# Kernel optimization log

Measured on AMD Instinct MI355X. Metric: run time of the kernel, lower is better.

The kernel has to match this reference:

```python
import jax, jax.numpy as jnp
import numpy as np

B, S, E, L = 4, 4096, 1024, 64
SCALE = float(np.sqrt(L))


def setup_inputs() -> dict:
    key = jax.random.key(0)
    ks = jax.random.split(key, 7)
    x = jax.random.normal(ks[0], (B, S, E), dtype=jnp.float32)
    # causal mask: positions with mask==0 are disallowed (masked_fill semantics)
    mask = jnp.tril(jnp.ones((S, S), dtype=jnp.int32))
    # Linear params (torch Linear: y = x @ W.T + b); store as [E, L] for x @ W
    sd = 1.0 / np.sqrt(E)
    Wq = jax.random.uniform(ks[1], (E, L), jnp.float32, -sd, sd)
    Wk = jax.random.uniform(ks[2], (E, L), jnp.float32, -sd, sd)
    Wv = jax.random.uniform(ks[3], (E, L), jnp.float32, -sd, sd)
    bq = jax.random.uniform(ks[4], (L,), jnp.float32, -sd, sd)
    bk = jax.random.uniform(ks[5], (L,), jnp.float32, -sd, sd)
    bv = jax.random.uniform(ks[6], (L,), jnp.float32, -sd, sd)
    return {"x": x, "Wq": Wq, "Wk": Wk, "Wv": Wv,
            "bq": bq, "bk": bk, "bv": bv, "mask": mask}


def reference(x, Wq, Wk, Wv, bq, bk, bv, mask):
    # Q,K,V: [B, S, L]
    Q = x @ Wq + bq
    K = x @ Wk + bk
    V = x @ Wv + bv
    # scores: [B, S, S] -- naive full matrix, faithful to the original
    scores = jnp.einsum('bsl,btl->bst', Q, K) / SCALE
    scores = jnp.where(mask == 0, -jnp.inf, scores)
    attn = jax.nn.softmax(scores, axis=-1)
    return jnp.einsum('bst,btl->bsl', attn, V)
```

## Files before the change

kernel.cpp:

```cpp
#include <hip/hip_runtime.h>
#include <hip/hip_bf16.h>
#include <cstdint>

typedef __bf16 bf16_t;
typedef __bf16 bf16x8 __attribute__((ext_vector_type(8)));
typedef float f32x4 __attribute__((ext_vector_type(4)));

#define B_ 4
#define S_ 4096
#define E_ 1024
#define L_ 64

__device__ __forceinline__ f32x4 mfma16(bf16x8 a, bf16x8 b, f32x4 c) {
  return __builtin_amdgcn_mfma_f32_16x16x32_bf16(a, b, c, 0, 0, 0);
}

template <int CTRL>
__device__ __forceinline__ float dpp_max_step(float x) {
  int t = __builtin_amdgcn_update_dpp(0, __float_as_int(x), CTRL, 0xF, 0xF, true);
  return fmaxf(x, __int_as_float(t));
}
template <int CTRL>
__device__ __forceinline__ float dpp_add_step(float x) {
  int t = __builtin_amdgcn_update_dpp(0, __float_as_int(x), CTRL, 0xF, 0xF, true);
  return x + __int_as_float(t);
}
__device__ __forceinline__ float dpp_reduce_max16(float x) {
  x = dpp_max_step<0x121>(x);
  x = dpp_max_step<0x122>(x);
  x = dpp_max_step<0x124>(x);
  x = dpp_max_step<0x128>(x);
  return x;
}
__device__ __forceinline__ float dpp_reduce_add16(float x) {
  x = dpp_add_step<0x121>(x);
  x = dpp_add_step<0x122>(x);
  x = dpp_add_step<0x124>(x);
  x = dpp_add_step<0x128>(x);
  return x;
}


__global__ void prep_w_kernel(const float* __restrict__ Wq, const float* __restrict__ Wk,
                              const float* __restrict__ Wv, bf16_t* __restrict__ Wf) {
  int n = blockIdx.x;
  const float* W = (n < 64) ? Wq : (n < 128 ? Wk : Wv);
  int col = n & 63;
  int nt = n >> 4, lr = n & 15;
  for (int k = threadIdx.x; k < E_; k += blockDim.x) {
    int kt = k >> 5, lg = (k >> 3) & 3, e = k & 7;
    Wf[((size_t)((nt * 32 + kt) * 64 + lg * 16 + lr) << 3) + e] = (bf16_t)W[(size_t)k * L_ + col];
  }
}

__global__ __launch_bounds__(512) void qkv_proj_kernel(
    const float* __restrict__ x, const bf16_t* __restrict__ Wf,
    const float* __restrict__ bq, const float* __restrict__ bk, const float* __restrict__ bv,
    bf16_t* __restrict__ Qf, bf16_t* __restrict__ Kf, bf16_t* __restrict__ Vf) {
  __shared__ __align__(16) bf16_t xbuf[2][64][136];
  bf16_t* stc = &xbuf[0][0][0];

  const int tid = threadIdx.x;
  const int w = tid >> 6, l = tid & 63;
  const int lr = l & 15, lg = l >> 4;
  const int rowgrp = w & 1, colgrp = w >> 1;
  const int m0 = blockIdx.x * 64;

  float4 ra[2], rb[2];
  int prow[2], pcol[2];
#pragma unroll
  for (int p = 0; p < 2; ++p) {
    const int g = p * 512 + tid;
    prow[p] = g >> 4;
    pcol[p] = (g & 15) * 8;
  }

#define QKV_LOADREG(c)                                                          \
  {                                                                             \
    _Pragma("unroll") for (int p = 0; p < 2; ++p) {                             \
      const float* src = x + (size_t)(m0 + prow[p]) * E_ + (c) * 128 + pcol[p]; \
      ra[p] = *reinterpret_cast<const float4*>(src);                            \
      rb[p] = *reinterpret_cast<const float4*>(src + 4);                        \
    }                                                                           \
  }
#define QKV_WRITE(b)                                                            \
  {                                                                             \
    _Pragma("unroll") for (int p = 0; p < 2; ++p) {                             \
      bf16x8 pk;                                                                \
      pk[0] = (bf16_t)ra[p].x; pk[1] = (bf16_t)ra[p].y;                         \
      pk[2] = (bf16_t)ra[p].z; pk[3] = (bf16_t)ra[p].w;                         \
      pk[4] = (bf16_t)rb[p].x; pk[5] = (bf16_t)rb[p].y;                         \
      pk[6] = (bf16_t)rb[p].z; pk[7] = (bf16_t)rb[p].w;                         \
      *reinterpret_cast<bf16x8*>(&xbuf[(b)][prow[p]][pcol[p]]) = pk;            \
    }                                                                           \
  }

  f32x4 acc[2][3];
#pragma unroll
  for (int rt = 0; rt < 2; ++rt)
#pragma unroll
    for (int t = 0; t < 3; ++t) acc[rt][t] = f32x4{0.f, 0.f, 0.f, 0.f};

  QKV_LOADREG(0);
  QKV_WRITE(0);
  QKV_LOADREG(1);
  __syncthreads();

  for (int c = 0; c < 8; ++c) {
    const int cur = c & 1;
#pragma unroll
    for (int kt = 0; kt < 4; ++kt) {
      const int ktg = c * 4 + kt;
      bf16x8 bfr[3];
#pragma unroll
      for (int t = 0; t < 3; ++t) {
        const int nt = colgrp * 3 + t;
        bfr[t] = *reinterpret_cast<const bf16x8*>(Wf + (((size_t)(nt * 32 + ktg) * 64 + l) << 3));
      }
#pragma unroll
      for (int rt = 0; rt < 2; ++rt) {
        bf16x8 a = *reinterpret_cast<const bf16x8*>(
            &xbuf[cur][rowgrp * 32 + rt * 16 + lr][kt * 32 + lg * 8]);
#pragma unroll
        for (int t = 0; t < 3; ++t) acc[rt][t] = mfma16(a, bfr[t], acc[rt][t]);
      }
    }
    if (c + 1 < 8) QKV_WRITE(cur ^ 1);
    if (c + 2 < 8) QKV_LOADREG(c + 2);
    __syncthreads();
  }

#pragma unroll
  for (int t = 0; t < 3; ++t) {
    const int colb = colgrp * 48 + t * 16;
    const int col = colb + lr;
    const int mat = colb >> 6;
    const float* bias = (mat == 0) ? bq : (mat == 1 ? bk : bv);
    const float bb = bias[col & 63];
#pragma unroll
    for (int rt = 0; rt < 2; ++rt)
#pragma unroll
      for (int r = 0; r < 4; ++r) {
        const int row = rowgrp * 32 + rt * 16 + lg * 4 + r;
        stc[row * 200 + col] = (bf16_t)(acc[rt][t][r] + bb);
      }
  }
  __syncthreads();

  {
    const int lane = tid & 63;
    const int lgw = lane >> 4, lrw = lane & 15;
    const int rt = tid >> 7, ktq = (tid >> 6) & 1;
    const int rtg = (m0 >> 4) + rt;
    bf16x8 qv = *reinterpret_cast<const bf16x8*>(stc + (rt * 16 + lrw) * 200 + ktq * 32 + lgw * 8);
    *reinterpret_cast<bf16x8*>(Qf + (((size_t)(rtg * 2 + ktq) * 64 + lane) << 3)) = qv;
    bf16x8 kv = *reinterpret_cast<const bf16x8*>(stc + (rt * 16 + lrw) * 200 + 64 + ktq * 32 + lgw * 8);
    *reinterpret_cast<bf16x8*>(Kf + (((size_t)(rtg * 2 + ktq) * 64 + lane) << 3)) = kv;
    const int stl = tid >> 8, vt = (tid >> 6) & 3;
    const int colv = vt * 16 + lrw;
    bf16x8 vv;
#pragma unroll
    for (int e = 0; e < 8; ++e)
      vv[e] = stc[(stl * 32 + lgw * 8 + e) * 200 + 128 + colv];
    const int batch = m0 >> 12;
    const int stg = ((m0 & (S_ - 1)) >> 5) + stl;
    *reinterpret_cast<bf16x8*>(Vf + ((size_t)batch << 18) + (((size_t)(stg * 4 + vt) * 64 + lane) << 3)) = vv;
  }
#undef QKV_LOADREG
#undef QKV_WRITE
}

__global__ __launch_bounds__(256) void attn_kernel(
    const bf16_t* __restrict__ Qf, const bf16_t* __restrict__ Kf,
    const bf16_t* __restrict__ Vf, float* __restrict__ Opart, float* __restrict__ mlpart) {
  __shared__ __align__(16) bf16_t p_lds[4][16 * 72];
  __shared__ bf16_t od_lds[3][16][68];
  __shared__ float ml_lds[3][16][2];

  const int c = threadIdx.x >> 6, l = threadIdx.x & 63;
  const int lr = l & 15, lg = l >> 4;
  const int u = blockIdx.x;
  const int batch = u & 3;
  const int strip = (u >> 2) & 3;
  const int h = (u >> 4) & 1;
  const int qt = 63 - (u >> 5);
  const int qsi = ((u >> 5) << 4) | (u & 15);
  const int qrow = qt * 64 + strip * 16;
  const size_t qbase = (size_t)batch * S_ + qrow;
  bf16_t* pw = p_lds[c];

  const int rtq = batch * 256 + qt * 4 + strip;
  bf16x8 qa0 = *reinterpret_cast<const bf16x8*>(Qf + (((size_t)(rtq * 2) * 64 + l) << 3));
  bf16x8 qa1 = *reinterpret_cast<const bf16x8*>(Qf + (((size_t)(rtq * 2 + 1) * 64 + l) << 3));
  const bf16_t* Vb = Vf + ((size_t)batch << 18);

  f32x4 o[4];
  float m[4], ssum[4];
#pragma unroll
  for (int rr = 0; rr < 4; ++rr) { o[rr] = f32x4{0.f, 0.f, 0.f, 0.f}; m[rr] = -1e30f; ssum[rr] = 0.f; }

  for (int kt = 2 * c + h; kt <= qt; kt += 8) {
    const int t0 = kt * 64;
    f32x4 st[4];
#pragma unroll
    for (int cf = 0; cf < 4; ++cf) st[cf] = f32x4{0.f, 0.f, 0.f, 0.f};
#pragma unroll
    for (int cf = 0; cf < 4; ++cf) {
      const int rtk = batch * 256 + kt * 4 + cf;
      bf16x8 b0 = *reinterpret_cast<const bf16x8*>(Kf + (((size_t)(rtk * 2) * 64 + l) << 3));
      bf16x8 b1 = *reinterpret_cast<const bf16x8*>(Kf + (((size_t)(rtk * 2 + 1) * 64 + l) << 3));
      st[cf] = mfma16(qa0, b0, st[cf]);
      st[cf] = mfma16(qa1, b1, st[cf]);
    }
    const bool diag = (kt == qt);
    float p[4][4];
#pragma unroll
    for (int rr = 0; rr < 4; ++rr) {
      const int qg = qrow + lg * 4 + rr;
      float rowmax = -1e30f;
#pragma unroll
      for (int cf = 0; cf < 4; ++cf) {
        float s = st[cf][rr] * 0.125f;
        if (diag && (t0 + cf * 16 + lr) > qg) s = -1e30f;
        p[cf][rr] = s;
        rowmax = fmaxf(rowmax, s);
      }
      rowmax = dpp_reduce_max16(rowmax);
      float mnew = fmaxf(m[rr], rowmax);
      float scale = __expf(m[rr] - mnew);
      float rs = 0.f;
#pragma unroll
      for (int cf = 0; cf < 4; ++cf) {
        float e = __expf(p[cf][rr] - mnew);
        p[cf][rr] = e;
        rs += e;
      }
      rs = dpp_reduce_add16(rs);
      ssum[rr] = ssum[rr] * scale + rs;
#pragma unroll
      for (int cf = 0; cf < 4; ++cf) o[cf][rr] *= scale;
      m[rr] = mnew;
    }
#pragma unroll
    for (int rr = 0; rr < 4; ++rr)
#pragma unroll
      for (int cf = 0; cf < 4; ++cf)
        pw[(lg * 4 + rr) * 72 + cf * 16 + lr] = (bf16_t)p[cf][rr];
    bf16x8 pa0 = *reinterpret_cast<const bf16x8*>(pw + lr * 72 + lg * 8);
    bf16x8 pa1 = *reinterpret_cast<const bf16x8*>(pw + lr * 72 + 32 + lg * 8);
    const int st0 = kt * 2;
#pragma unroll
    for (int cf = 0; cf < 4; ++cf) {
      bf16x8 v0 = *reinterpret_cast<const bf16x8*>(Vb + (((size_t)((st0 * 4 + cf) * 64 + l)) << 3));
      bf16x8 v1 = *reinterpret_cast<const bf16x8*>(Vb + (((size_t)(((st0 + 1) * 4 + cf) * 64 + l)) << 3));
      o[cf] = mfma16(pa0, v0, o[cf]);
      o[cf] = mfma16(pa1, v1, o[cf]);
    }
  }

  if (c > 0) {
    if (lr == 0) {
#pragma unroll
      for (int rr = 0; rr < 4; ++rr) {
        ml_lds[c - 1][lg * 4 + rr][0] = m[rr];
        ml_lds[c - 1][lg * 4 + rr][1] = ssum[rr];
      }
    }
#pragma unroll
    for (int cf = 0; cf < 4; ++cf)
#pragma unroll
      for (int rr = 0; rr < 4; ++rr)
        od_lds[c - 1][lg * 4 + rr][cf * 16 + lr] = (bf16_t)o[cf][rr];
  }
  __syncthreads();
  if (c == 0) {
    float* Op = Opart + (size_t)(h * 1024 + qsi) * 1024;
    float* mlp = mlpart + (size_t)(h * 1024 + qsi) * 32;
#pragma unroll
    for (int rr = 0; rr < 4; ++rr) {
      const int row = lg * 4 + rr;
      float M = m[rr];
      float mv[3];
#pragma unroll
      for (int cc = 0; cc < 3; ++cc) {
        mv[cc] = ml_lds[cc][row][0];
        M = fmaxf(M, mv[cc]);
      }
      float f0 = __expf(m[rr] - M);
      float Lsum = ssum[rr] * f0;
      float fc[3];
#pragma unroll
      for (int cc = 0; cc < 3; ++cc) {
        fc[cc] = __expf(mv[cc] - M);
        Lsum += ml_lds[cc][row][1] * fc[cc];
      }
      if (lr == 0) { mlp[row * 2] = M; mlp[row * 2 + 1] = Lsum; }
#pragma unroll
      for (int cf = 0; cf < 4; ++cf) {
        float val = o[cf][rr] * f0;
#pragma unroll
        for (int cc = 0; cc < 3; ++cc)
          val += (float)od_lds[cc][row][cf * 16 + lr] * fc[cc];
        Op[row * 64 + cf * 16 + lr] = val;
      }
    }
  }
}

__global__ __launch_bounds__(64) void combine_kernel(
    const float* __restrict__ Opart, const float* __restrict__ mlpart,
    float* __restrict__ out) {
  const int b = blockIdx.x;
  const int batch = b & 3, strip = (b >> 2) & 3, qt = 63 - (b >> 4);
  const int l = threadIdx.x;
  const int row = l >> 2, c0 = (l & 3) * 16;
  const float* ml0 = mlpart + ((size_t)(0 * 1024 + b) * 16 + row) * 2;
  const float* ml1 = mlpart + ((size_t)(1 * 1024 + b) * 16 + row) * 2;
  float m0 = ml0[0], l0 = ml0[1], m1 = ml1[0], l1 = ml1[1];
  float M = fmaxf(m0, m1);
  float f0 = __expf(m0 - M), f1 = __expf(m1 - M);
  float inv = 1.f / (l0 * f0 + l1 * f1);
  const float* O0 = Opart + (size_t)(0 * 1024 + b) * 1024 + row * 64 + c0;
  const float* O1 = Opart + (size_t)(1 * 1024 + b) * 1024 + row * 64 + c0;
  float* dst = out + ((size_t)batch * S_ + qt * 64 + strip * 16 + row) * L_ + c0;
#pragma unroll
  for (int j = 0; j < 4; ++j) {
    float4 a = reinterpret_cast<const float4*>(O0)[j];
    float4 bb = reinterpret_cast<const float4*>(O1)[j];
    float4 v;
    v.x = (a.x * f0 + bb.x * f1) * inv;
    v.y = (a.y * f0 + bb.y * f1) * inv;
    v.z = (a.z * f0 + bb.z * f1) * inv;
    v.w = (a.w * f0 + bb.w * f1) * inv;
    reinterpret_cast<float4*>(dst)[j] = v;
  }
}

extern "C" void kernel_launch(void* const* d_in, const int* in_sizes, int n_in,
                              void* d_out, int out_size, void* d_ws, size_t ws_size,
                              hipStream_t stream) {
  (void)in_sizes; (void)n_in; (void)out_size; (void)ws_size;
  const float* x  = (const float*)d_in[0];
  const float* Wq = (const float*)d_in[1];
  const float* Wk = (const float*)d_in[2];
  const float* Wv = (const float*)d_in[3];
  const float* bq = (const float*)d_in[4];
  const float* bk = (const float*)d_in[5];
  const float* bv = (const float*)d_in[6];
  float* out = (float*)d_out;

  char* ws = (char*)d_ws;
  bf16_t* Qf  = (bf16_t*)(ws + 0);
  bf16_t* Kf  = (bf16_t*)(ws + (size_t)2 * 1024 * 1024);
  bf16_t* Vf  = (bf16_t*)(ws + (size_t)4 * 1024 * 1024);
  bf16_t* Wf  = (bf16_t*)(ws + (size_t)6 * 1024 * 1024);
  float* Opart = (float*)(ws + (size_t)7 * 1024 * 1024);
  float* mlpart = (float*)(ws + (size_t)15 * 1024 * 1024);

  hipLaunchKernelGGL(prep_w_kernel, dim3(192), dim3(256), 0, stream, Wq, Wk, Wv, Wf);
  hipLaunchKernelGGL(qkv_proj_kernel, dim3(16384 / 64), dim3(512), 0, stream,
                     x, Wf, bq, bk, bv, Qf, Kf, Vf);
  hipLaunchKernelGGL(attn_kernel, dim3(2048), dim3(256), 0, stream,
                     Qf, Kf, Vf, Opart, mlpart);
  hipLaunchKernelGGL(combine_kernel, dim3(1024), dim3(64), 0, stream,
                     Opart, mlpart, out);
}
```

Measured before the change: 61.26 us.

## Store normalized partial outputs in bf16 and rotate QKV K-chunk order

The attention kernel now normalizes each half's partial output by its own softmax sum and stores it as bf16 rather than fp32. This halves Opart write and read traffic, and the combine kernel becomes a weighted blend of the two halves. Separately, the QKV projection rotates the order in which each block walks the E dimension, spreading concurrent blocks across different columns of x and Wf. The bf16 partials reduce output precision somewhat.

```diff
diff --git a/kernel.cpp b/kernel.cpp
--- a/kernel.cpp
+++ b/kernel.cpp
@@ -65,6 +65,7 @@
   const int lr = l & 15, lg = l >> 4;
   const int rowgrp = w & 1, colgrp = w >> 1;
   const int m0 = blockIdx.x * 64;
+  const int rot = blockIdx.x & 7;
 
   float4 ra[2], rb[2];
   int prow[2], pcol[2];
@@ -75,10 +76,12 @@
     pcol[p] = (g & 15) * 8;
   }
 
+#define QKV_CC(c) (((c) + rot) & 7)
 #define QKV_LOADREG(c)                                                          \
   {                                                                             \
+    const int cc_ = QKV_CC(c);                                                  \
     _Pragma("unroll") for (int p = 0; p < 2; ++p) {                             \
-      const float* src = x + (size_t)(m0 + prow[p]) * E_ + (c) * 128 + pcol[p]; \
+      const float* src = x + (size_t)(m0 + prow[p]) * E_ + cc_ * 128 + pcol[p]; \
       ra[p] = *reinterpret_cast<const float4*>(src);                            \
       rb[p] = *reinterpret_cast<const float4*>(src + 4);                        \
     }                                                                           \
@@ -108,9 +111,10 @@
 
   for (int c = 0; c < 8; ++c) {
     const int cur = c & 1;
+    const int cc = QKV_CC(c);
 #pragma unroll
     for (int kt = 0; kt < 4; ++kt) {
-      const int ktg = c * 4 + kt;
+      const int ktg = cc * 4 + kt;
       bf16x8 bfr[3];
 #pragma unroll
       for (int t = 0; t < 3; ++t) {
@@ -166,13 +170,14 @@
     const int stg = ((m0 & (S_ - 1)) >> 5) + stl;
     *reinterpret_cast<bf16x8*>(Vf + ((size_t)batch << 18) + (((size_t)(stg * 4 + vt) * 64 + lane) << 3)) = vv;
   }
+#undef QKV_CC
 #undef QKV_LOADREG
 #undef QKV_WRITE
 }
 
 __global__ __launch_bounds__(256) void attn_kernel(
     const bf16_t* __restrict__ Qf, const bf16_t* __restrict__ Kf,
-    const bf16_t* __restrict__ Vf, float* __restrict__ Opart, float* __restrict__ mlpart) {
+    const bf16_t* __restrict__ Vf, bf16_t* __restrict__ Opart, float* __restrict__ mlpart) {
   __shared__ __align__(16) bf16_t p_lds[4][16 * 72];
   __shared__ bf16_t od_lds[3][16][68];
   __shared__ float ml_lds[3][16][2];
@@ -274,7 +279,7 @@
   }
   __syncthreads();
   if (c == 0) {
-    float* Op = Opart + (size_t)(h * 1024 + qsi) * 1024;
+    bf16_t* Op = Opart + (size_t)(h * 1024 + qsi) * 1024;
     float* mlp = mlpart + (size_t)(h * 1024 + qsi) * 32;
 #pragma unroll
     for (int rr = 0; rr < 4; ++rr) {
@@ -294,6 +299,7 @@
         fc[cc] = __expf(mv[cc] - M);
         Lsum += ml_lds[cc][row][1] * fc[cc];
       }
+      const float invL = (Lsum > 0.f) ? (1.f / Lsum) : 0.f;
       if (lr == 0) { mlp[row * 2] = M; mlp[row * 2 + 1] = Lsum; }
 #pragma unroll
       for (int cf = 0; cf < 4; ++cf) {
@@ -301,14 +307,14 @@
 #pragma unroll
         for (int cc = 0; cc < 3; ++cc)
           val += (float)od_lds[cc][row][cf * 16 + lr] * fc[cc];
-        Op[row * 64 + cf * 16 + lr] = val;
+        Op[row * 64 + cf * 16 + lr] = (bf16_t)(val * invL);
       }
     }
   }
 }
 
 __global__ __launch_bounds__(64) void combine_kernel(
-    const float* __restrict__ Opart, const float* __restrict__ mlpart,
+    const bf16_t* __restrict__ Opart, const float* __restrict__ mlpart,
     float* __restrict__ out) {
   const int b = blockIdx.x;
   const int batch = b & 3, strip = (b >> 2) & 3, qt = 63 - (b >> 4);
@@ -318,21 +324,19 @@
   const float* ml1 = mlpart + ((size_t)(1 * 1024 + b) * 16 + row) * 2;
   float m0 = ml0[0], l0 = ml0[1], m1 = ml1[0], l1 = ml1[1];
   float M = fmaxf(m0, m1);
-  float f0 = __expf(m0 - M), f1 = __expf(m1 - M);
-  float inv = 1.f / (l0 * f0 + l1 * f1);
-  const float* O0 = Opart + (size_t)(0 * 1024 + b) * 1024 + row * 64 + c0;
-  const float* O1 = Opart + (size_t)(1 * 1024 + b) * 1024 + row * 64 + c0;
+  float w0 = l0 * __expf(m0 - M), w1 = l1 * __expf(m1 - M);
+  float inv = 1.f / (w0 + w1);
+  w0 *= inv; w1 *= inv;
+  const bf16_t* O0 = Opart + (size_t)(0 * 1024 + b) * 1024 + row * 64 + c0;
+  const bf16_t* O1 = Opart + (size_t)(1 * 1024 + b) * 1024 + row * 64 + c0;
   float* dst = out + ((size_t)batch * S_ + qt * 64 + strip * 16 + row) * L_ + c0;
 #pragma unroll
-  for (int j = 0; j < 4; ++j) {
-    float4 a = reinterpret_cast<const float4*>(O0)[j];
-    float4 bb = reinterpret_cast<const float4*>(O1)[j];
-    float4 v;
-    v.x = (a.x * f0 + bb.x * f1) * inv;
-    v.y = (a.y * f0 + bb.y * f1) * inv;
-    v.z = (a.z * f0 + bb.z * f1) * inv;
-    v.w = (a.w * f0 + bb.w * f1) * inv;
-    reinterpret_cast<float4*>(dst)[j] = v;
+  for (int j = 0; j < 2; ++j) {
+    bf16x8 a = reinterpret_cast<const bf16x8*>(O0)[j];
+    bf16x8 bb = reinterpret_cast<const bf16x8*>(O1)[j];
+#pragma unroll
+    for (int e = 0; e < 8; ++e)
+      dst[j * 8 + e] = (float)a[e] * w0 + (float)bb[e] * w1;
   }
 }
 
@@ -354,8 +358,8 @@
   bf16_t* Kf  = (bf16_t*)(ws + (size_t)2 * 1024 * 1024);
   bf16_t* Vf  = (bf16_t*)(ws + (size_t)4 * 1024 * 1024);
   bf16_t* Wf  = (bf16_t*)(ws + (size_t)6 * 1024 * 1024);
-  float* Opart = (float*)(ws + (size_t)7 * 1024 * 1024);
-  float* mlpart = (float*)(ws + (size_t)15 * 1024 * 1024);
+  bf16_t* Opart = (bf16_t*)(ws + (size_t)7 * 1024 * 1024);
+  float* mlpart = (float*)(ws + (size_t)12 * 1024 * 1024);
 
   hipLaunchKernelGGL(prep_w_kernel, dim3(192), dim3(256), 0, stream, Wq, Wk, Wv, Wf);
   hipLaunchKernelGGL(qkv_proj_kernel, dim3(16384 / 64), dim3(512), 0, stream,
```

New measurement: 59.13 us. 1.04x faster.
